# Optimization experiments

Hardware: AMD Instinct MI355X
Metric: run time of the kernel (lower is better)

The kernel has to match this reference:

```python
import jax, jax.numpy as jnp
import numpy as np

BN_EPS = 1e-3  # Keras BatchNormalization default epsilon


def setup_inputs() -> dict:
    key = jax.random.key(0)
    ks = jax.random.split(key, 16)
    B, N, M = 4, 16384, 4096
    C1, C2 = 128, 256
    mlp = [256, 128]
    cin = C2 + C1
    inp = {
        "xyz1": jax.random.normal(ks[0], (B, N, 3), dtype=jnp.float32),
        "xyz2": jax.random.normal(ks[1], (B, M, 3), dtype=jnp.float32),
        "points1": jax.random.normal(ks[2], (B, N, C1), dtype=jnp.float32),
        "points2": jax.random.normal(ks[3], (B, M, C2), dtype=jnp.float32),
    }
    k = 4
    for i, cout in enumerate(mlp):
        inp[f"w{i}"] = jax.random.normal(ks[k], (cin, cout), dtype=jnp.float32) * (1.0 / np.sqrt(cin)); k += 1
        inp[f"g{i}"] = jnp.ones((cout,), dtype=jnp.float32) + 0.1 * jax.random.normal(ks[k], (cout,), dtype=jnp.float32); k += 1
        inp[f"b{i}"] = 0.1 * jax.random.normal(ks[k], (cout,), dtype=jnp.float32); k += 1
        inp[f"m{i}"] = 0.1 * jax.random.normal(ks[k], (cout,), dtype=jnp.float32); k += 1
        inp[f"v{i}"] = 0.5 + jax.random.uniform(ks[k], (cout,), dtype=jnp.float32); k += 1
        cin = cout
    return inp


def _three_nn(xyz1, xyz2):
    # squared pairwise distances [B,N,M] via ||a||^2 + ||b||^2 - 2ab
    n1 = jnp.sum(xyz1 * xyz1, axis=-1)                      # [B,N]
    n2 = jnp.sum(xyz2 * xyz2, axis=-1)                      # [B,M]
    d2 = n1[:, :, None] + n2[:, None, :] - 2.0 * jnp.einsum("bnc,bmc->bnm", xyz1, xyz2)
    d2 = jnp.maximum(d2, 0.0)
    neg, idx = jax.lax.top_k(-d2, 3)                        # 3 smallest distances
    return -neg, idx                                        # dist [B,N,3], idx [B,N,3]


def reference(xyz1, xyz2, points1, points2,
              w0, g0, b0, m0, v0, w1, g1, b1, m1, v1):
    dist, idx = _three_nn(xyz1, xyz2)
    dist = jnp.maximum(dist, 1e-10)
    inv = 1.0 / dist                                        # [B,N,3]
    weight = inv / jnp.sum(inv, axis=2, keepdims=True)      # [B,N,3]
    # three_interpolate: irregular gather + weighted sum
    gathered = jax.vmap(lambda p, i: p[i])(points2, idx)    # [B,N,3,C2]
    interp = jnp.einsum("bnk,bnkc->bnc", weight, gathered)  # [B,N,C2]
    x = jnp.concatenate([interp, points1], axis=2)          # [B,N,C2+C1]
    # 1x1 Conv2D (no bias) + BN(inference) + ReLU stack
    for w, g, b, m, v in ((w0, g0, b0, m0, v0), (w1, g1, b1, m1, v1)):
        x = jnp.einsum("bnc,cd->bnd", x, w)
        x = (x - m) * (g * jax.lax.rsqrt(v + BN_EPS)) + b
        x = jax.nn.relu(x)
    return x
```

## Files before the change

kernel.cpp:

```cpp
#include <hip/hip_runtime.h>
#include <hip/hip_bf16.h>

typedef __bf16 bf16x8 __attribute__((ext_vector_type(8)));
typedef float  f32x4  __attribute__((ext_vector_type(4)));
typedef unsigned short ushort_t;
typedef unsigned int   uint_t;

__device__ __forceinline__ ushort_t f2bf(float f) {
    union { float f; uint_t u; } v; v.f = f;
    uint_t r = v.u + 0x7fffu + ((v.u >> 16) & 1u);
    return (ushort_t)(r >> 16);
}

#define BATCH 4
#define NPTS  16384
#define MPTS  4096
#define C1    128
#define C2    256
#define NCHUNK 4
#define CHUNK  (MPTS / NCHUNK)

__global__ __launch_bounds__(256) void prep_kernel(
    const float* __restrict__ w0, const float* __restrict__ w1,
    const float* __restrict__ g0, const float* __restrict__ b0,
    const float* __restrict__ m0, const float* __restrict__ v0,
    const float* __restrict__ g1, const float* __restrict__ b1,
    const float* __restrict__ m1, const float* __restrict__ v1,
    ushort_t* __restrict__ wt0, ushort_t* __restrict__ wt1,
    float* __restrict__ sc0, float* __restrict__ sh0,
    float* __restrict__ sc1, float* __restrict__ sh1) {
    int i = blockIdx.x * 256 + threadIdx.x;
    if (i < 256 * 384) {
        int n = i / 384, k = i % 384;
        wt0[i] = f2bf(w0[k * 256 + n]);
    }
    if (i < 128 * 256) {
        int n = i / 256, k = i % 256;
        wt1[i] = f2bf(w1[k * 128 + n]);
    }
    if (i < 256) { float s = g0[i] * rsqrtf(v0[i] + 1e-3f); sc0[i] = s; sh0[i] = b0[i] - m0[i] * s; }
    if (i < 128) { float s = g1[i] * rsqrtf(v1[i] + 1e-3f); sc1[i] = s; sh1[i] = b1[i] - m1[i] * s; }
}

__global__ __launch_bounds__(256) void knn_partial(
    const float* __restrict__ xyz1, const float* __restrict__ xyz2,
    float* __restrict__ pd, int* __restrict__ pi) {
    __shared__ __align__(16) float sx[CHUNK], sy_[CHUNK], sz[CHUNK], sw[CHUNK];
    const int t  = threadIdx.x;
    const int qb = blockIdx.x;
    const int c  = blockIdx.y;
    const int b  = blockIdx.z;
#pragma unroll
    for (int j = 0; j < CHUNK / 256; j++) {
        const int m = j * 256 + t;
        const float* g = xyz2 + ((long)b * MPTS + c * CHUNK + m) * 3;
        const float x = g[0], y = g[1], z = g[2];
        sx[m] = x; sy_[m] = y; sz[m] = z; sw[m] = x * x + y * y + z * z;
    }
    __syncthreads();
    const int n = qb * 256 + t;
    const long base = ((long)b * NPTS + n) * 3;
    const float qx = xyz1[base], qy = xyz1[base + 1], qz = xyz1[base + 2];
    const float nx = -2.f * qx, ny = -2.f * qy, nz = -2.f * qz;
    float d0 = 3.4e38f, d1 = 3.4e38f, d2 = 3.4e38f;
    int   i0 = 0, i1 = 0, i2 = 0;
    const int mb = c * CHUNK;
    for (int g = 0; g < CHUNK; g += 4) {
        const float4 X = *(const float4*)&sx[g];
        const float4 Y = *(const float4*)&sy_[g];
        const float4 Z = *(const float4*)&sz[g];
        const float4 W = *(const float4*)&sw[g];
        const float xs[4] = {X.x, X.y, X.z, X.w};
        const float ys[4] = {Y.x, Y.y, Y.z, Y.w};
        const float zs[4] = {Z.x, Z.y, Z.z, Z.w};
        const float ws[4] = {W.x, W.y, W.z, W.w};
#pragma unroll
        for (int j = 0; j < 4; j++) {
            const float s = fmaf(xs[j], nx, fmaf(ys[j], ny, fmaf(zs[j], nz, ws[j])));
            const bool c2 = s < d2;
            if (__ballot(c2)) {
                const int m = mb + g + j;
                const bool c0 = s < d0, c1 = s < d1;
                const int ni2 = c1 ? i1 : (c2 ? m : i2);
                const int ni1 = c0 ? i0 : (c1 ? m : i1);
                const int ni0 = c0 ? m : i0;
                const float nd0 = fminf(d0, s);
                const float nd1 = __builtin_amdgcn_fmed3f(d0, d1, s);
                const float nd2 = __builtin_amdgcn_fmed3f(d1, d2, s);
                d0 = nd0; d1 = nd1; d2 = nd2;
                i0 = ni0; i1 = ni1; i2 = ni2;
            }
        }
    }
    const long po = ((long)c * (BATCH * NPTS) + (long)b * NPTS + n) * 3;
    pd[po] = d0; pd[po + 1] = d1; pd[po + 2] = d2;
    pi[po] = i0; pi[po + 1] = i1; pi[po + 2] = i2;
}

__global__ __launch_bounds__(256) void knn_merge(
    const float* __restrict__ xyz1,
    const float* __restrict__ pd, const int* __restrict__ pi,
    int* __restrict__ idx, float* __restrict__ wgt) {
    const long n = blockIdx.x * 256 + threadIdx.x;
    float d0 = 3.4e38f, d1 = 3.4e38f, d2 = 3.4e38f;
    int   i0 = 0, i1 = 0, i2 = 0;
#pragma unroll
    for (int c = 0; c < NCHUNK; c++) {
        const long po = ((long)c * (BATCH * NPTS) + n) * 3;
#pragma unroll
        for (int k = 0; k < 3; k++) {
            const float d = pd[po + k];
            const int   m = pi[po + k];
            const bool c0 = d < d0, c1 = d < d1, c2 = d < d2;
            const float nd2 = c1 ? d1 : (c2 ? d : d2);
            const int   ni2 = c1 ? i1 : (c2 ? m : i2);
            const float nd1 = c0 ? d0 : (c1 ? d : d1);
            const int   ni1 = c0 ? i0 : (c1 ? m : i1);
            d0 = c0 ? d : d0;  i0 = c0 ? m : i0;
            d1 = nd1; i1 = ni1; d2 = nd2; i2 = ni2;
        }
    }
    const float qx = xyz1[n * 3], qy = xyz1[n * 3 + 1], qz = xyz1[n * 3 + 2];
    const float qn = qx * qx + qy * qy + qz * qz;
    d0 = fmaxf(d0 + qn, 1e-10f);
    d1 = fmaxf(d1 + qn, 1e-10f);
    d2 = fmaxf(d2 + qn, 1e-10f);
    const float w0 = 1.f / d0, w1 = 1.f / d1, w2 = 1.f / d2;
    const float rs = 1.f / (w0 + w1 + w2);
    const long o = n * 3;
    idx[o] = i0; idx[o + 1] = i1; idx[o + 2] = i2;
    wgt[o] = w0 * rs; wgt[o + 1] = w1 * rs; wgt[o + 2] = w2 * rs;
}

#define XT_STRIDE 392
#define SY_STRIDE 264
__global__ __launch_bounds__(256) void mlp_fused(
    const float* __restrict__ points1, const float* __restrict__ points2,
    const int* __restrict__ idx, const float* __restrict__ wgt,
    const ushort_t* __restrict__ Bt0,
    const ushort_t* __restrict__ Bt1,
    const float* __restrict__ sc0, const float* __restrict__ sh0,
    const float* __restrict__ sc1, const float* __restrict__ sh1,
    float* __restrict__ outp) {
    __shared__ ushort_t xt[32 * XT_STRIDE];
    __shared__ ushort_t sy[32 * SY_STRIDE];
    const int tid = threadIdx.x;
    const int wv = tid >> 6, lane = tid & 63;
    const int q = lane >> 4, l16 = lane & 15;
    const int rowBase = blockIdx.x * 32;
    const int b = rowBase >> 14;

#pragma unroll
    for (int rr = 0; rr < 8; rr++) {
        const int row = wv * 8 + rr;
        const long o = (long)(rowBase + row) * 3;
        int i0 = idx[o], i1 = idx[o + 1], i2 = idx[o + 2];
        i0 = min(max(i0, 0), MPTS - 1);
        i1 = min(max(i1, 0), MPTS - 1);
        i2 = min(max(i2, 0), MPTS - 1);
        const float w0 = wgt[o], w1 = wgt[o + 1], w2 = wgt[o + 2];
        const float4* p0 = (const float4*)(points2 + ((long)b * MPTS + i0) * C2);
        const float4* p1 = (const float4*)(points2 + ((long)b * MPTS + i1) * C2);
        const float4* p2 = (const float4*)(points2 + ((long)b * MPTS + i2) * C2);
        const float4 a = p0[lane], bb = p1[lane], cc = p2[lane];
        ushort4 u;
        u.x = f2bf(w0 * a.x + w1 * bb.x + w2 * cc.x);
        u.y = f2bf(w0 * a.y + w1 * bb.y + w2 * cc.y);
        u.z = f2bf(w0 * a.z + w1 * bb.z + w2 * cc.z);
        u.w = f2bf(w0 * a.w + w1 * bb.w + w2 * cc.w);
        *(ushort4*)((char*)xt + row * (XT_STRIDE * 2) + lane * 8) = u;
        const float2* qp = (const float2*)(points1 + (long)(rowBase + row) * C1);
        const float2 tq = qp[lane];
        const uint_t packed = (uint_t)f2bf(tq.x) | ((uint_t)f2bf(tq.y) << 16);
        *(uint_t*)((char*)xt + row * (XT_STRIDE * 2) + 512 + lane * 4) = packed;
    }
    __syncthreads();

    const int wcol = wv * 64;
    f32x4 acc[2][4] = {};
#pragma unroll 2
    for (int step = 0; step < 12; step++) {
        const int kk = step * 32;
        bf16x8 af[2], bfr[4];
#pragma unroll
        for (int t = 0; t < 2; t++)
            af[t] = *(const bf16x8*)((const char*)xt + (t * 16 + l16) * (XT_STRIDE * 2) + kk * 2 + q * 16);
#pragma unroll
        for (int t = 0; t < 4; t++) {
            const int col = wcol + t * 16 + l16;
            bfr[t] = *(const bf16x8*)(Bt0 + (long)col * 384 + kk + q * 8);
        }
#pragma unroll
        for (int tr = 0; tr < 2; tr++)
#pragma unroll
            for (int tc = 0; tc < 4; tc++)
                acc[tr][tc] = __builtin_amdgcn_mfma_f32_16x16x32_bf16(af[tr], bfr[tc], acc[tr][tc], 0, 0, 0);
    }
#pragma unroll
    for (int tc = 0; tc < 4; tc++) {
        const int ycol = wcol + tc * 16 + l16;
        const float sc = sc0[ycol], sh = sh0[ycol];
#pragma unroll
        for (int tr = 0; tr < 2; tr++) {
#pragma unroll
            for (int r = 0; r < 4; r++) {
                const int row0 = tr * 16 + q * 4 + r;
                sy[row0 * SY_STRIDE + ycol] = f2bf(fmaxf(acc[tr][tc][r] * sc + sh, 0.f));
            }
        }
    }
    __syncthreads();

    const int wcol2 = wv * 32;
    f32x4 acc2[2][2] = {};
#pragma unroll 2
    for (int step = 0; step < 8; step++) {
        const int kk = step * 32;
        bf16x8 af2[2], bf2[2];
#pragma unroll
        for (int t = 0; t < 2; t++)
            af2[t] = *(const bf16x8*)((const char*)sy + (t * 16 + l16) * (SY_STRIDE * 2) + kk * 2 + q * 16);
#pragma unroll
        for (int t = 0; t < 2; t++) {
            const int col = wcol2 + t * 16 + l16;
            bf2[t] = *(const bf16x8*)(Bt1 + (long)col * 256 + kk + q * 8);
        }
#pragma unroll
        for (int tr = 0; tr < 2; tr++)
#pragma unroll
            for (int tc = 0; tc < 2; tc++)
                acc2[tr][tc] = __builtin_amdgcn_mfma_f32_16x16x32_bf16(af2[tr], bf2[tc], acc2[tr][tc], 0, 0, 0);
    }
#pragma unroll
    for (int tc = 0; tc < 2; tc++) {
        const int col = wcol2 + tc * 16 + l16;
        const float sc = sc1[col], sh = sh1[col];
#pragma unroll
        for (int tr = 0; tr < 2; tr++) {
#pragma unroll
            for (int r = 0; r < 4; r++) {
                const int row = rowBase + tr * 16 + q * 4 + r;
                outp[(long)row * 128 + col] = fmaxf(acc2[tr][tc][r] * sc + sh, 0.f);
            }
        }
    }
}

extern "C" void kernel_launch(void* const* d_in, const int* in_sizes, int n_in,
                              void* d_out, int out_size, void* d_ws, size_t ws_size,
                              hipStream_t stream) {
    const float* xyz1    = (const float*)d_in[0];
    const float* xyz2    = (const float*)d_in[1];
    const float* points1 = (const float*)d_in[2];
    const float* points2 = (const float*)d_in[3];
    const float* w0 = (const float*)d_in[4];
    const float* g0 = (const float*)d_in[5];
    const float* b0 = (const float*)d_in[6];
    const float* m0 = (const float*)d_in[7];
    const float* v0 = (const float*)d_in[8];
    const float* w1 = (const float*)d_in[9];
    const float* g1 = (const float*)d_in[10];
    const float* b1 = (const float*)d_in[11];
    const float* m1 = (const float*)d_in[12];
    const float* v1 = (const float*)d_in[13];

    char* ws = (char*)d_ws;
    int*      idx = (int*)ws;
    float*    wgt = (float*)(ws + 786432);
    ushort_t* wt0 = (ushort_t*)(ws + 1572864);
    ushort_t* wt1 = (ushort_t*)(ws + 1769472);
    float*    sc0 = (float*)(ws + 1835008);
    float*    sh0 = sc0 + 256;
    float*    sc1 = sh0 + 256;
    float*    sh1 = sc1 + 128;
    float* pd = (float*)(ws + 2097152);
    int*   pi = (int*)(ws + 2097152 + 6291456);

    prep_kernel<<<384, 256, 0, stream>>>(w0, w1, g0, b0, m0, v0, g1, b1, m1, v1,
                                         wt0, wt1, sc0, sh0, sc1, sh1);
    knn_partial<<<dim3(NPTS / 256, NCHUNK, BATCH), 256, 0, stream>>>(xyz1, xyz2, pd, pi);
    knn_merge<<<(BATCH * NPTS) / 256, 256, 0, stream>>>(xyz1, pd, pi, idx, wgt);
    mlp_fused<<<(BATCH * NPTS) / 32, 256, 0, stream>>>(
        points1, points2, idx, wgt, wt0, wt1, sc0, sh0, sc1, sh1, (float*)d_out);
}
```

Measured before the change: 269.6 us.

## Enlarge MLP row tile to 64 with 2x2 warp layout, XOR swizzle, register prefetch

The fused MLP kernel now handles 64 rows per block instead of 32, using a 2x2 wave layout where each wave owns a 32x128 (then 32x64) output tile. This halves how often each block reloads the weight fragments from global memory. Padded LDS strides are replaced with an XOR swizzle on a single shared buffer that is reused for both layers. Both GEMM loops also double-buffer A/B fragments in registers. In exchange, more accumulators raise register pressure and the grid has half as many blocks, which can lower occupancy.

```diff
diff --git a/kernel.cpp b/kernel.cpp
--- a/kernel.cpp
+++ b/kernel.cpp
@@ -132,8 +132,6 @@
     wgt[o] = w0 * rs; wgt[o + 1] = w1 * rs; wgt[o + 2] = w2 * rs;
 }
 
-#define XT_STRIDE 392
-#define SY_STRIDE 264
 __global__ __launch_bounds__(256) void mlp_fused(
     const float* __restrict__ points1, const float* __restrict__ points2,
     const int* __restrict__ idx, const float* __restrict__ wgt,
@@ -142,17 +140,16 @@
     const float* __restrict__ sc0, const float* __restrict__ sh0,
     const float* __restrict__ sc1, const float* __restrict__ sh1,
     float* __restrict__ outp) {
-    __shared__ ushort_t xt[32 * XT_STRIDE];
-    __shared__ ushort_t sy[32 * SY_STRIDE];
+    __shared__ __align__(16) char smem[64 * 768];
     const int tid = threadIdx.x;
     const int wv = tid >> 6, lane = tid & 63;
     const int q = lane >> 4, l16 = lane & 15;
-    const int rowBase = blockIdx.x * 32;
+    const int rowBase = blockIdx.x * 64;
     const int b = rowBase >> 14;
 
-#pragma unroll
-    for (int rr = 0; rr < 8; rr++) {
-        const int row = wv * 8 + rr;
+#pragma unroll 4
+    for (int rr = 0; rr < 16; rr++) {
+        const int row = wv * 16 + rr;
         const long o = (long)(rowBase + row) * 3;
         int i0 = idx[o], i1 = idx[o + 1], i2 = idx[o + 2];
         i0 = min(max(i0, 0), MPTS - 1);
@@ -168,78 +165,120 @@
         u.y = f2bf(w0 * a.y + w1 * bb.y + w2 * cc.y);
         u.z = f2bf(w0 * a.z + w1 * bb.z + w2 * cc.z);
         u.w = f2bf(w0 * a.w + w1 * bb.w + w2 * cc.w);
-        *(ushort4*)((char*)xt + row * (XT_STRIDE * 2) + lane * 8) = u;
+        const int sw = (row & 7) << 4;
+        *(ushort4*)(smem + row * 768 + ((lane * 8) ^ sw)) = u;
         const float2* qp = (const float2*)(points1 + (long)(rowBase + row) * C1);
         const float2 tq = qp[lane];
         const uint_t packed = (uint_t)f2bf(tq.x) | ((uint_t)f2bf(tq.y) << 16);
-        *(uint_t*)((char*)xt + row * (XT_STRIDE * 2) + 512 + lane * 4) = packed;
+        *(uint_t*)(smem + row * 768 + ((512 + lane * 4) ^ sw)) = packed;
     }
     __syncthreads();
 
-    const int wcol = wv * 64;
-    f32x4 acc[2][4] = {};
-#pragma unroll 2
+    const int wr = (wv & 1) * 32;
+    const int wc = (wv >> 1) * 128;
+    f32x4 acc[2][8] = {};
+    bf16x8 aC[2], bC[8];
+#pragma unroll
+    for (int t = 0; t < 2; t++) {
+        const int row = wr + t * 16 + l16;
+        aC[t] = *(const bf16x8*)(smem + row * 768 + ((q * 16) ^ ((row & 7) << 4)));
+    }
+#pragma unroll
+    for (int t = 0; t < 8; t++)
+        bC[t] = *(const bf16x8*)(Bt0 + (long)(wc + t * 16 + l16) * 384 + q * 8);
+#pragma unroll
     for (int step = 0; step < 12; step++) {
-        const int kk = step * 32;
-        bf16x8 af[2], bfr[4];
-#pragma unroll
-        for (int t = 0; t < 2; t++)
-            af[t] = *(const bf16x8*)((const char*)xt + (t * 16 + l16) * (XT_STRIDE * 2) + kk * 2 + q * 16);
-#pragma unroll
-        for (int t = 0; t < 4; t++) {
-            const int col = wcol + t * 16 + l16;
-            bfr[t] = *(const bf16x8*)(Bt0 + (long)col * 384 + kk + q * 8);
+        bf16x8 aN[2], bN[8];
+        if (step < 11) {
+            const int koff = (step + 1) * 64 + q * 16;
+            const int kk = (step + 1) * 32;
+#pragma unroll
+            for (int t = 0; t < 2; t++) {
+                const int row = wr + t * 16 + l16;
+                aN[t] = *(const bf16x8*)(smem + row * 768 + (koff ^ ((row & 7) << 4)));
+            }
+#pragma unroll
+            for (int t = 0; t < 8; t++)
+                bN[t] = *(const bf16x8*)(Bt0 + (long)(wc + t * 16 + l16) * 384 + kk + q * 8);
         }
 #pragma unroll
         for (int tr = 0; tr < 2; tr++)
 #pragma unroll
+            for (int tc = 0; tc < 8; tc++)
+                acc[tr][tc] = __builtin_amdgcn_mfma_f32_16x16x32_bf16(aC[tr], bC[tc], acc[tr][tc], 0, 0, 0);
+        if (step < 11) {
+#pragma unroll
+            for (int t = 0; t < 2; t++) aC[t] = aN[t];
+#pragma unroll
+            for (int t = 0; t < 8; t++) bC[t] = bN[t];
+        }
+    }
+    __syncthreads();
+
+#pragma unroll
+    for (int tc = 0; tc < 8; tc++) {
+        const int col = wc + tc * 16 + l16;
+        const float sc = sc0[col], sh = sh0[col];
+#pragma unroll
+        for (int tr = 0; tr < 2; tr++) {
+#pragma unroll
+            for (int r = 0; r < 4; r++) {
+                const int row = wr + tr * 16 + q * 4 + r;
+                const ushort_t hv = f2bf(fmaxf(acc[tr][tc][r] * sc + sh, 0.f));
+                *(ushort_t*)(smem + row * 512 + ((col * 2) ^ ((row & 7) << 4))) = hv;
+            }
+        }
+    }
+    __syncthreads();
+
+    const int wc2 = (wv >> 1) * 64;
+    f32x4 acc2[2][4] = {};
+    bf16x8 a2[2], b2[4];
+#pragma unroll
+    for (int t = 0; t < 2; t++) {
+        const int row = wr + t * 16 + l16;
+        a2[t] = *(const bf16x8*)(smem + row * 512 + ((q * 16) ^ ((row & 7) << 4)));
+    }
+#pragma unroll
+    for (int t = 0; t < 4; t++)
+        b2[t] = *(const bf16x8*)(Bt1 + (long)(wc2 + t * 16 + l16) * 256 + q * 8);
+#pragma unroll
+    for (int step = 0; step < 8; step++) {
+        bf16x8 aN[2], bN[4];
+        if (step < 7) {
+            const int koff = (step + 1) * 64 + q * 16;
+            const int kk = (step + 1) * 32;
+#pragma unroll
+            for (int t = 0; t < 2; t++) {
+                const int row = wr + t * 16 + l16;
+                aN[t] = *(const bf16x8*)(smem + row * 512 + (koff ^ ((row & 7) << 4)));
+            }
+#pragma unroll
+            for (int t = 0; t < 4; t++)
+                bN[t] = *(const bf16x8*)(Bt1 + (long)(wc2 + t * 16 + l16) * 256 + kk + q * 8);
+        }
+#pragma unroll
+        for (int tr = 0; tr < 2; tr++)
+#pragma unroll
             for (int tc = 0; tc < 4; tc++)
-                acc[tr][tc] = __builtin_amdgcn_mfma_f32_16x16x32_bf16(af[tr], bfr[tc], acc[tr][tc], 0, 0, 0);
-    }
+                acc2[tr][tc] = __builtin_amdgcn_mfma_f32_16x16x32_bf16(a2[tr], b2[tc], acc2[tr][tc], 0, 0, 0);
+        if (step < 7) {
+#pragma unroll
+            for (int t = 0; t < 2; t++) a2[t] = aN[t];
+#pragma unroll
+            for (int t = 0; t < 4; t++) b2[t] = bN[t];
+        }
+    }
+
 #pragma unroll
     for (int tc = 0; tc < 4; tc++) {
-        const int ycol = wcol + tc * 16 + l16;
-        const float sc = sc0[ycol], sh = sh0[ycol];
+        const int col = wc2 + tc * 16 + l16;
+        const float sc = sc1[col], sh = sh1[col];
 #pragma unroll
         for (int tr = 0; tr < 2; tr++) {
 #pragma unroll
             for (int r = 0; r < 4; r++) {
-                const int row0 = tr * 16 + q * 4 + r;
-                sy[row0 * SY_STRIDE + ycol] = f2bf(fmaxf(acc[tr][tc][r] * sc + sh, 0.f));
-            }
-        }
-    }
-    __syncthreads();
-
-    const int wcol2 = wv * 32;
-    f32x4 acc2[2][2] = {};
-#pragma unroll 2
-    for (int step = 0; step < 8; step++) {
-        const int kk = step * 32;
-        bf16x8 af2[2], bf2[2];
-#pragma unroll
-        for (int t = 0; t < 2; t++)
-            af2[t] = *(const bf16x8*)((const char*)sy + (t * 16 + l16) * (SY_STRIDE * 2) + kk * 2 + q * 16);
-#pragma unroll
-        for (int t = 0; t < 2; t++) {
-            const int col = wcol2 + t * 16 + l16;
-            bf2[t] = *(const bf16x8*)(Bt1 + (long)col * 256 + kk + q * 8);
-        }
-#pragma unroll
-        for (int tr = 0; tr < 2; tr++)
-#pragma unroll
-            for (int tc = 0; tc < 2; tc++)
-                acc2[tr][tc] = __builtin_amdgcn_mfma_f32_16x16x32_bf16(af2[tr], bf2[tc], acc2[tr][tc], 0, 0, 0);
-    }
-#pragma unroll
-    for (int tc = 0; tc < 2; tc++) {
-        const int col = wcol2 + tc * 16 + l16;
-        const float sc = sc1[col], sh = sh1[col];
-#pragma unroll
-        for (int tr = 0; tr < 2; tr++) {
-#pragma unroll
-            for (int r = 0; r < 4; r++) {
-                const int row = rowBase + tr * 16 + q * 4 + r;
+                const int row = rowBase + wr + tr * 16 + q * 4 + r;
                 outp[(long)row * 128 + col] = fmaxf(acc2[tr][tc][r] * sc + sh, 0.f);
             }
         }
@@ -280,6 +319,6 @@
                                          wt0, wt1, sc0, sh0, sc1, sh1);
     knn_partial<<<dim3(NPTS / 256, NCHUNK, BATCH), 256, 0, stream>>>(xyz1, xyz2, pd, pi);
     knn_merge<<<(BATCH * NPTS) / 256, 256, 0, stream>>>(xyz1, pd, pi, idx, wgt);
-    mlp_fused<<<(BATCH * NPTS) / 32, 256, 0, stream>>>(
+    mlp_fused<<<(BATCH * NPTS) / 64, 256, 0, stream>>>(
         points1, points2, idx, wgt, wt0, wt1, sc0, sh0, sc1, sh1, (float*)d_out);
 }
```

New measurement: 276.6 us. 2.6% more time.
